# Kernel tuning notes

Hardware: AMD Instinct MI355X
Metric: run time of the kernel (lower is better)

Reference implementation:

```python
import jax, jax.numpy as jnp
import numpy as np
from jax import lax

B, N, T, H, E, D, K = 2, 1024, 4096, 256, 2, 2, 9


def angle2vector(a):
    return jnp.stack([jnp.sin(a), jnp.cos(a)], axis=-1)


def setup_inputs() -> dict:
    key = jax.random.key(0)
    ks = jax.random.split(key, 16)
    s = jnp.float32(0.05)
    return {
        "x": jax.random.normal(ks[0], (B, N, T), jnp.float32),
        "z": jax.random.uniform(ks[1], (B, T, E, D), jnp.float32, 0.0, 2.0 * np.pi),
        # encoder: depthwise conv (groups=N) then two 1x1 convs
        "dw_w": jax.random.normal(ks[2], (N, 1, K), jnp.float32) * s,
        "dw_b": jax.random.normal(ks[3], (N,), jnp.float32) * s,
        "w1": jax.random.normal(ks[4], (H, N), jnp.float32) * s,
        "b1": jax.random.normal(ks[5], (H,), jnp.float32) * s,
        "w2": jax.random.normal(ks[6], (H, H), jnp.float32) * s,
        "b2": jax.random.normal(ks[7], (H,), jnp.float32) * s,
        # heads (1x1 convs)
        "wm": jax.random.normal(ks[8], (E * D * 2, H), jnp.float32) * s,
        "bm": jax.random.normal(ks[9], (E * D * 2,), jnp.float32) * s,
        "wv": jax.random.normal(ks[10], (E * D, H), jnp.float32) * s,
        "bv": jax.random.normal(ks[11], (E * D,), jnp.float32) * s,
        # feature basis / readout params
        "receptive_fields": jax.random.uniform(ks[12], (N, E, D), jnp.float32, 0.0, 2.0 * np.pi),
        "ensemble_weights": jax.random.normal(ks[13], (N, E), jnp.float32),
        "final_scale": jax.random.normal(ks[14], (N,), jnp.float32) * s,
        "log_tuning_width": jnp.full((1,), np.log(2.0), jnp.float32),
    }


def reference(x, z, dw_w, dw_b, w1, b1, w2, b2, wm, bm, wv, bv,
              receptive_fields, ensemble_weights, final_scale, log_tuning_width):
    # ---- encoder ----
    # depthwise conv1d, kernel_size=K, padding='same', groups=N
    h = lax.conv_general_dilated(
        x, dw_w, window_strides=(1,), padding="SAME",
        feature_group_count=N, dimension_numbers=("NCH", "OIH", "NCH"))
    h = h + dw_b[None, :, None]
    h = jax.nn.relu(jnp.einsum("hn,bnt->bht", w1, h) + b1[None, :, None])
    h = jax.nn.relu(jnp.einsum("gh,bht->bgt", w2, h) + b2[None, :, None])

    # ---- heads ----
    mu = jnp.einsum("oh,bht->bot", wm, h) + bm[None, :, None]  # [B, E*D*2, T]
    mu = mu.transpose(0, 2, 1).reshape(B, T, E, D, 2)
    logvar = jnp.einsum("oh,bht->bot", wv, h) + bv[None, :, None]  # [B, E*D, T]
    logvar = logvar.transpose(0, 2, 1).reshape(B, T, E, D)
    # normalize encodings onto unit circle
    mu = mu / jnp.sqrt(jnp.sum(mu ** 2, axis=-1, keepdims=True))

    # ---- feature basis ('bump') ----
    zv = angle2vector(z)                     # [B, T, E, D, 2]
    rfv = angle2vector(receptive_fields)     # [N, E, D, 2]
    diff = zv[:, :, None] - rfv[None, None]  # [B, T, N, E, D, 2]
    dist = jnp.sum(diff ** 2, axis=(4, 5))   # [B, T, N, E]
    response = jnp.exp(-dist / jnp.exp(log_tuning_width))  # nonlinearity='exp'

    # ---- ensemble-weighted readout ----
    ew = jax.nn.softmax(ensemble_weights, axis=1)  # [N, E]
    responses = jnp.einsum("btne,ne->btn", response, ew)
    responses = responses * jnp.exp(final_scale)[None, None]
    responses = responses.transpose(0, 2, 1)  # [B, N, T]
    return responses, z, mu, logvar
```

## Files before the change

### kernel.cpp

```cpp
#include <hip/hip_runtime.h>
#include <hip/hip_bf16.h>

#define B_ 2
#define N_ 1024
#define T_ 4096
#define H_ 256
#define ROWS_ 8192

typedef float f32x4 __attribute__((ext_vector_type(4)));
typedef __bf16 bf16x8 __attribute__((ext_vector_type(8)));

__device__ __forceinline__ void gl16(const void* g, void* l) {
  __builtin_amdgcn_global_load_lds(
      (const __attribute__((address_space(1))) void*)g,
      (__attribute__((address_space(3))) void*)l, 16, 0, 0);
}

__global__ __launch_bounds__(256) void cvt_split(
    const float* __restrict__ w1, const float* __restrict__ w2,
    __bf16* __restrict__ w1h, __bf16* __restrict__ w1l,
    __bf16* __restrict__ w2h, __bf16* __restrict__ w2l) {
  int i = blockIdx.x * 256 + threadIdx.x;
  if (i < 262144) {
    float v = w1[i];
    __bf16 h = (__bf16)v;
    w1h[i] = h;
    w1l[i] = (__bf16)(v - (float)h);
  } else {
    int j = i - 262144;
    float v = w2[j];
    __bf16 h = (__bf16)v;
    w2h[j] = h;
    w2l[j] = (__bf16)(v - (float)h);
  }
}

__global__ __launch_bounds__(256) void dwconv_t(
    const float* __restrict__ x, const float* __restrict__ w,
    const float* __restrict__ bias, __bf16* __restrict__ h0h,
    __bf16* __restrict__ h0l) {
  __shared__ float xs[64][76];
  const int tid = threadIdx.x;
  const int t0 = blockIdx.x * 64;
  const int n0 = blockIdx.y * 64;
  const int b = blockIdx.z;
  for (int i = tid; i < 64 * 72; i += 256) {
    int rr = i / 72, cc = i % 72;
    int tt = t0 - 4 + cc;
    xs[rr][cc] = (tt >= 0 && tt < T_) ? x[((size_t)(b * N_ + n0 + rr)) * T_ + tt] : 0.f;
  }
  const int nl = tid & 63;
  const int tg = tid >> 6;
  float wr[9];
  #pragma unroll
  for (int k = 0; k < 9; ++k) wr[k] = w[(n0 + nl) * 9 + k];
  const float bb = bias[n0 + nl];
  __syncthreads();
  float win[24];
  #pragma unroll
  for (int c = 0; c < 6; ++c)
    *(f32x4*)&win[c * 4] = *(const f32x4*)&xs[nl][tg * 16 + c * 4];
  const size_t obase = ((size_t)b * T_ + t0 + tg * 16) * N_ + n0 + nl;
  #pragma unroll
  for (int j = 0; j < 16; ++j) {
    float acc = bb;
    #pragma unroll
    for (int k = 0; k < 9; ++k) acc = fmaf(win[j + k], wr[k], acc);
    __bf16 h = (__bf16)acc;
    h0h[obase + (size_t)j * N_] = h;
    h0l[obase + (size_t)j * N_] = (__bf16)(acc - (float)h);
  }
}

__global__ __launch_bounds__(256) void gemm3p(
    const __bf16* __restrict__ Ah, const __bf16* __restrict__ Al,
    const __bf16* __restrict__ Wh, const __bf16* __restrict__ Wl,
    const float* __restrict__ bias, __bf16* __restrict__ Oh,
    __bf16* __restrict__ Ol, int K, int relu) {
  __shared__ __bf16 As[2][2][64 * 32];
  __shared__ __bf16 Ws[2][2][64 * 32];
  const int tid = threadIdx.x;
  const int orig = blockIdx.x;
  const int rm = (orig & 7) * 64 + (orig >> 3);
  const int g0 = (rm & 3) * 64;
  const int row0 = (rm >> 2) * 64;

  const int sr = tid >> 2;
  const int sl = tid & 3;
  const int ssl = sl ^ ((sr >> 1) & 3);
  const size_t a_off = (size_t)(row0 + sr) * K + ssl * 8;
  const size_t w_off = (size_t)(g0 + sr) * K + ssl * 8;

  const int lane = tid & 63;
  const int wid = tid >> 6;
  const int wrr = (wid >> 1) * 32;
  const int wcc = (wid & 1) * 32;
  const int lr = lane & 15;
  const int ls = lane >> 4;

  f32x4 acc[2][2];
  #pragma unroll
  for (int i = 0; i < 2; ++i)
    #pragma unroll
    for (int j = 0; j < 2; ++j) acc[i][j] = (f32x4)0.f;

  auto STAGE = [&](int buf, int k0) {
    gl16(Ah + a_off + k0, &As[buf][0][tid * 8]);
    gl16(Al + a_off + k0, &As[buf][1][tid * 8]);
    gl16(Wh + w_off + k0, &Ws[buf][0][tid * 8]);
    gl16(Wl + w_off + k0, &Ws[buf][1][tid * 8]);
  };

  auto FADDR = [&](int r) { return r * 32 + (ls ^ ((r >> 1) & 3)) * 8; };

  const int nk = K >> 5;
  STAGE(0, 0);
  __syncthreads();
  for (int kt = 0; kt < nk; ++kt) {
    const int cur = kt & 1;
    if (kt + 1 < nk) STAGE(cur ^ 1, (kt + 1) << 5);
    bf16x8 ah[2], al[2], wh[2], wl[2];
    #pragma unroll
    for (int mi = 0; mi < 2; ++mi) {
      int a = FADDR(wrr + mi * 16 + lr);
      ah[mi] = *(const bf16x8*)&As[cur][0][a];
      al[mi] = *(const bf16x8*)&As[cur][1][a];
    }
    #pragma unroll
    for (int ni = 0; ni < 2; ++ni) {
      int a = FADDR(wcc + ni * 16 + lr);
      wh[ni] = *(const bf16x8*)&Ws[cur][0][a];
      wl[ni] = *(const bf16x8*)&Ws[cur][1][a];
    }
    #pragma unroll
    for (int mi = 0; mi < 2; ++mi)
      #pragma unroll
      for (int ni = 0; ni < 2; ++ni) {
        acc[mi][ni] = __builtin_amdgcn_mfma_f32_16x16x32_bf16(ah[mi], wh[ni], acc[mi][ni], 0, 0, 0);
        acc[mi][ni] = __builtin_amdgcn_mfma_f32_16x16x32_bf16(ah[mi], wl[ni], acc[mi][ni], 0, 0, 0);
        acc[mi][ni] = __builtin_amdgcn_mfma_f32_16x16x32_bf16(al[mi], wh[ni], acc[mi][ni], 0, 0, 0);
      }
    __syncthreads();
  }

  #pragma unroll
  for (int ni = 0; ni < 2; ++ni) {
    const int g = g0 + wcc + ni * 16 + lr;
    const float bb = bias[g];
    #pragma unroll
    for (int mi = 0; mi < 2; ++mi)
      #pragma unroll
      for (int reg = 0; reg < 4; ++reg) {
        int t = row0 + wrr + mi * 16 + ls * 4 + reg;
        float v = acc[mi][ni][reg] + bb;
        if (relu) v = fmaxf(v, 0.f);
        __bf16 h = (__bf16)v;
        Oh[(size_t)t * H_ + g] = h;
        Ol[(size_t)t * H_ + g] = (__bf16)(v - (float)h);
      }
  }
}

__global__ __launch_bounds__(256) void heads_t(
    const __bf16* __restrict__ h2h, const __bf16* __restrict__ h2l,
    const float* __restrict__ wm, const float* __restrict__ bm,
    const float* __restrict__ wv, const float* __restrict__ bv,
    float* __restrict__ out_mu, float* __restrict__ out_lv) {
  __shared__ float sw[12][256];
  const int tid = threadIdx.x;
  for (int i = tid; i < 8 * 256; i += 256) sw[i >> 8][i & 255] = wm[i];
  for (int i = tid; i < 4 * 256; i += 256) sw[8 + (i >> 8)][i & 255] = wv[i];
  __syncthreads();
  const int tq = tid & 3;
  const int tl = tid >> 2;
  const size_t row = blockIdx.x * 64 + tl;
  float s[12];
  #pragma unroll
  for (int o = 0; o < 12; ++o) s[o] = 0.f;
  for (int j = 0; j < 8; ++j) {
    int jj = (j + tq * 2) & 7;
    int k0 = tq * 64 + jj * 8;
    bf16x8 vh = *(const bf16x8*)&h2h[row * 256 + k0];
    bf16x8 vl = *(const bf16x8*)&h2l[row * 256 + k0];
    #pragma unroll
    for (int e = 0; e < 8; ++e) {
      float v = (float)vh[e] + (float)vl[e];
      #pragma unroll
      for (int o = 0; o < 12; ++o) s[o] = fmaf(sw[o][k0 + e], v, s[o]);
    }
  }
  #pragma unroll
  for (int o = 0; o < 12; ++o) {
    s[o] += __shfl_xor(s[o], 1);
    s[o] += __shfl_xor(s[o], 2);
  }
  if (tq == 0) {
    float mm[8];
    #pragma unroll
    for (int ed = 0; ed < 4; ++ed) {
      float m0 = s[ed * 2] + bm[ed * 2];
      float m1 = s[ed * 2 + 1] + bm[ed * 2 + 1];
      float inv = 1.f / sqrtf(m0 * m0 + m1 * m1);
      mm[ed * 2] = m0 * inv;
      mm[ed * 2 + 1] = m1 * inv;
    }
    *(float4*)&out_mu[row * 8] = make_float4(mm[0], mm[1], mm[2], mm[3]);
    *(float4*)&out_mu[row * 8 + 4] = make_float4(mm[4], mm[5], mm[6], mm[7]);
  } else if (tq == 1) {
    *(float4*)&out_lv[row * 4] =
        make_float4(s[8] + bv[0], s[9] + bv[1], s[10] + bv[2], s[11] + bv[3]);
  }
}

__global__ __launch_bounds__(256) void resp_kernel(
    const float* __restrict__ z, const float* __restrict__ rf,
    const float* __restrict__ ew, const float* __restrict__ fs,
    const float* __restrict__ ltw, float* __restrict__ out,
    float* __restrict__ out_z) {
  __shared__ float s_sin[64][4];
  __shared__ float s_cos[64][4];
  __shared__ float s_w[64][2];
  const int tid = threadIdx.x;
  const int tc = blockIdx.x;
  const int nc = blockIdx.y;
  const int b = blockIdx.z;
  {
    int nl = tid >> 2, ed = tid & 3;
    float a = rf[(nc * 64 + nl) * 4 + ed];
    s_sin[nl][ed] = sinf(a);
    s_cos[nl][ed] = cosf(a);
  }
  if (tid < 64) {
    int n = nc * 64 + tid;
    float e0 = ew[n * 2], e1 = ew[n * 2 + 1];
    float m = fmaxf(e0, e1);
    float x0 = expf(e0 - m), x1 = expf(e1 - m);
    float sc = expf(fs[n]) / (x0 + x1);
    s_w[tid][0] = x0 * sc;
    s_w[tid][1] = x1 * sc;
  }
  __syncthreads();
  const int t = tc * 256 + tid;
  const float inv_tw = expf(-ltw[0]);
  float4 zv = *(const float4*)&z[((size_t)b * T_ + t) * 4];
  if (nc == 0) *(float4*)&out_z[((size_t)b * T_ + t) * 4] = zv;
  float sz0 = sinf(zv.x), cz0 = cosf(zv.x);
  float sz1 = sinf(zv.y), cz1 = cosf(zv.y);
  float sz2 = sinf(zv.z), cz2 = cosf(zv.z);
  float sz3 = sinf(zv.w), cz3 = cosf(zv.w);
  float* op = out + (size_t)b * N_ * T_ + (size_t)(nc * 64) * T_ + t;
  #pragma unroll 4
  for (int nl = 0; nl < 64; ++nl) {
    float dot0 = sz0 * s_sin[nl][0] + cz0 * s_cos[nl][0] +
                 sz1 * s_sin[nl][1] + cz1 * s_cos[nl][1];
    float dot1 = sz2 * s_sin[nl][2] + cz2 * s_cos[nl][2] +
                 sz3 * s_sin[nl][3] + cz3 * s_cos[nl][3];
    float r0 = __expf((2.f * dot0 - 4.f) * inv_tw);
    float r1 = __expf((2.f * dot1 - 4.f) * inv_tw);
    op[(size_t)nl * T_] = s_w[nl][0] * r0 + s_w[nl][1] * r1;
  }
}

extern "C" void kernel_launch(void* const* d_in, const int* in_sizes, int n_in,
                              void* d_out, int out_size, void* d_ws, size_t ws_size,
                              hipStream_t stream) {
  const float* x   = (const float*)d_in[0];
  const float* z   = (const float*)d_in[1];
  const float* dww = (const float*)d_in[2];
  const float* dwb = (const float*)d_in[3];
  const float* w1  = (const float*)d_in[4];
  const float* b1  = (const float*)d_in[5];
  const float* w2  = (const float*)d_in[6];
  const float* b2  = (const float*)d_in[7];
  const float* wm  = (const float*)d_in[8];
  const float* bm  = (const float*)d_in[9];
  const float* wv  = (const float*)d_in[10];
  const float* bv  = (const float*)d_in[11];
  const float* rf  = (const float*)d_in[12];
  const float* ew  = (const float*)d_in[13];
  const float* fs  = (const float*)d_in[14];
  const float* ltw = (const float*)d_in[15];

  float* out = (float*)d_out;
  float* out_resp = out;
  float* out_z    = out + (size_t)B_ * N_ * T_;
  float* out_mu   = out_z + (size_t)B_ * T_ * 4;
  float* out_lv   = out_mu + (size_t)B_ * T_ * 8;

  __bf16* h0h = (__bf16*)out_resp;
  __bf16* h0l = h0h + (size_t)ROWS_ * N_;

  __bf16* p = (__bf16*)d_ws;
  __bf16* w1h = p; p += 262144;
  __bf16* w1l = p; p += 262144;
  __bf16* w2h = p; p += 65536;
  __bf16* w2l = p; p += 65536;
  __bf16* h1h = p; p += (size_t)ROWS_ * H_;
  __bf16* h1l = p; p += (size_t)ROWS_ * H_;
  __bf16* h2h = p; p += (size_t)ROWS_ * H_;
  __bf16* h2l = p; p += (size_t)ROWS_ * H_;

  cvt_split<<<1280, 256, 0, stream>>>(w1, w2, w1h, w1l, w2h, w2l);
  dwconv_t<<<dim3(T_ / 64, N_ / 64, B_), 256, 0, stream>>>(x, dww, dwb, h0h, h0l);
  gemm3p<<<dim3(512), 256, 0, stream>>>(h0h, h0l, w1h, w1l, b1, h1h, h1l, N_, 1);
  gemm3p<<<dim3(512), 256, 0, stream>>>(h1h, h1l, w2h, w2l, b2, h2h, h2l, H_, 1);
  heads_t<<<dim3(ROWS_ / 64), 256, 0, stream>>>(
      h2h, h2l, wm, bm, wv, bv, out_mu, out_lv);
  resp_kernel<<<dim3(T_ / 256, N_ / 64, B_), 256, 0, stream>>>(
      z, rf, ew, fs, ltw, out_resp, out_z);
}
```

Before: 183.0 us.

## Fuse both encoder GEMMs and heads into one kernel; vectorize response stores

After: 186.4 us. No clear change (+1.9%).

```diff
diff --git a/kernel.cpp b/kernel.cpp
--- a/kernel.cpp
+++ b/kernel.cpp
@@ -72,129 +72,170 @@
   }
 }
 
-__global__ __launch_bounds__(256) void gemm3p(
+__global__ __launch_bounds__(512) void encoder_fused(
     const __bf16* __restrict__ Ah, const __bf16* __restrict__ Al,
-    const __bf16* __restrict__ Wh, const __bf16* __restrict__ Wl,
-    const float* __restrict__ bias, __bf16* __restrict__ Oh,
-    __bf16* __restrict__ Ol, int K, int relu) {
-  __shared__ __bf16 As[2][2][64 * 32];
-  __shared__ __bf16 Ws[2][2][64 * 32];
-  const int tid = threadIdx.x;
-  const int orig = blockIdx.x;
-  const int rm = (orig & 7) * 64 + (orig >> 3);
-  const int g0 = (rm & 3) * 64;
-  const int row0 = (rm >> 2) * 64;
-
-  const int sr = tid >> 2;
-  const int sl = tid & 3;
-  const int ssl = sl ^ ((sr >> 1) & 3);
-  const size_t a_off = (size_t)(row0 + sr) * K + ssl * 8;
-  const size_t w_off = (size_t)(g0 + sr) * K + ssl * 8;
-
-  const int lane = tid & 63;
-  const int wid = tid >> 6;
-  const int wrr = (wid >> 1) * 32;
-  const int wcc = (wid & 1) * 32;
-  const int lr = lane & 15;
-  const int ls = lane >> 4;
-
-  f32x4 acc[2][2];
-  #pragma unroll
-  for (int i = 0; i < 2; ++i)
-    #pragma unroll
-    for (int j = 0; j < 2; ++j) acc[i][j] = (f32x4)0.f;
-
-  auto STAGE = [&](int buf, int k0) {
-    gl16(Ah + a_off + k0, &As[buf][0][tid * 8]);
-    gl16(Al + a_off + k0, &As[buf][1][tid * 8]);
-    gl16(Wh + w_off + k0, &Ws[buf][0][tid * 8]);
-    gl16(Wl + w_off + k0, &Ws[buf][1][tid * 8]);
-  };
-
-  auto FADDR = [&](int r) { return r * 32 + (ls ^ ((r >> 1) & 3)) * 8; };
-
-  const int nk = K >> 5;
-  STAGE(0, 0);
-  __syncthreads();
-  for (int kt = 0; kt < nk; ++kt) {
-    const int cur = kt & 1;
-    if (kt + 1 < nk) STAGE(cur ^ 1, (kt + 1) << 5);
-    bf16x8 ah[2], al[2], wh[2], wl[2];
-    #pragma unroll
-    for (int mi = 0; mi < 2; ++mi) {
-      int a = FADDR(wrr + mi * 16 + lr);
-      ah[mi] = *(const bf16x8*)&As[cur][0][a];
-      al[mi] = *(const bf16x8*)&As[cur][1][a];
-    }
-    #pragma unroll
-    for (int ni = 0; ni < 2; ++ni) {
-      int a = FADDR(wcc + ni * 16 + lr);
-      wh[ni] = *(const bf16x8*)&Ws[cur][0][a];
-      wl[ni] = *(const bf16x8*)&Ws[cur][1][a];
-    }
-    #pragma unroll
-    for (int mi = 0; mi < 2; ++mi)
-      #pragma unroll
-      for (int ni = 0; ni < 2; ++ni) {
-        acc[mi][ni] = __builtin_amdgcn_mfma_f32_16x16x32_bf16(ah[mi], wh[ni], acc[mi][ni], 0, 0, 0);
-        acc[mi][ni] = __builtin_amdgcn_mfma_f32_16x16x32_bf16(ah[mi], wl[ni], acc[mi][ni], 0, 0, 0);
-        acc[mi][ni] = __builtin_amdgcn_mfma_f32_16x16x32_bf16(al[mi], wh[ni], acc[mi][ni], 0, 0, 0);
-      }
-    __syncthreads();
-  }
-
-  #pragma unroll
-  for (int ni = 0; ni < 2; ++ni) {
-    const int g = g0 + wcc + ni * 16 + lr;
-    const float bb = bias[g];
-    #pragma unroll
-    for (int mi = 0; mi < 2; ++mi)
-      #pragma unroll
-      for (int reg = 0; reg < 4; ++reg) {
-        int t = row0 + wrr + mi * 16 + ls * 4 + reg;
-        float v = acc[mi][ni][reg] + bb;
-        if (relu) v = fmaxf(v, 0.f);
-        __bf16 h = (__bf16)v;
-        Oh[(size_t)t * H_ + g] = h;
-        Ol[(size_t)t * H_ + g] = (__bf16)(v - (float)h);
-      }
-  }
-}
-
-__global__ __launch_bounds__(256) void heads_t(
-    const __bf16* __restrict__ h2h, const __bf16* __restrict__ h2l,
+    const __bf16* __restrict__ W1h, const __bf16* __restrict__ W1l,
+    const float* __restrict__ b1,
+    const __bf16* __restrict__ W2h, const __bf16* __restrict__ W2l,
+    const float* __restrict__ b2,
     const float* __restrict__ wm, const float* __restrict__ bm,
     const float* __restrict__ wv, const float* __restrict__ bv,
     float* __restrict__ out_mu, float* __restrict__ out_lv) {
-  __shared__ float sw[12][256];
+  __shared__ __attribute__((aligned(16))) char smem[126976];
+  char* const ASB = smem;
+  char* const WSB = smem + 8192;
+  char* const H1B = smem + 73728;
+  float* const WMV = (float*)(smem + 106496);
+  float* const H2S = (float*)(smem + 8192);
+
   const int tid = threadIdx.x;
-  for (int i = tid; i < 8 * 256; i += 256) sw[i >> 8][i & 255] = wm[i];
-  for (int i = tid; i < 4 * 256; i += 256) sw[8 + (i >> 8)][i & 255] = wv[i];
-  __syncthreads();
-  const int tq = tid & 3;
-  const int tl = tid >> 2;
-  const size_t row = blockIdx.x * 64 + tl;
+  const int row0 = blockIdx.x * 32;
+  const int lane = tid & 63;
+  const int wid = tid >> 6;
+  const int wt = (wid >> 2) * 16;
+  const int wg = (wid & 3) * 64;
+  const int lr = lane & 15;
+  const int ls = lane >> 4;
+
+  if (tid < 256) {
+    #pragma unroll
+    for (int i = 0; i < 8; ++i) WMV[tid * 20 + i] = wm[i * 256 + tid];
+    #pragma unroll
+    for (int i = 0; i < 4; ++i) WMV[tid * 20 + 8 + i] = wv[i * 256 + tid];
+  }
+
+  float b1g[4], b2g[4];
+  #pragma unroll
+  for (int ni = 0; ni < 4; ++ni) {
+    b1g[ni] = b1[wg + ni * 16 + lr];
+    b2g[ni] = b2[wg + ni * 16 + lr];
+  }
+
+  const int a_pl = tid >> 7;
+  const int a_idx = tid & 127;
+  const int a_r = a_idx >> 2;
+  const int a_c = (a_idx & 3) ^ ((a_r >> 1) & 3);
+  const __bf16* a_src = (a_pl ? Al : Ah) + (size_t)(row0 + a_r) * 1024 + a_c * 8;
+  char* const a_dst = ASB + a_pl * 2048 + a_idx * 16;
+
+  auto STAGE_A = [&](int buf, int kt) {
+    if (tid < 256) gl16(a_src + kt * 32, a_dst + buf * 4096);
+  };
+  auto STAGE_W = [&](int buf, int k0, const __bf16* Wh, const __bf16* Wl, int K) {
+    #pragma unroll
+    for (int j = 0; j < 4; ++j) {
+      const int s = tid + j * 512;
+      const int pl = s >> 10;
+      const int idx = s & 1023;
+      const int g = idx >> 2;
+      const int c = (idx & 3) ^ ((g >> 1) & 3);
+      gl16((pl ? Wl : Wh) + (size_t)g * K + k0 + c * 8, WSB + buf * 32768 + s * 16);
+    }
+  };
+  auto FR_A = [&](int cur, int pl, int r) {
+    return *(const bf16x8*)(ASB + cur * 4096 + pl * 2048 + r * 64 +
+                            (ls ^ ((r >> 1) & 3)) * 16);
+  };
+  auto FR_W = [&](int cur, int pl, int g) {
+    return *(const bf16x8*)(WSB + cur * 32768 + pl * 16384 + g * 64 +
+                            (ls ^ ((g >> 1) & 3)) * 16);
+  };
+
+  f32x4 acc[4];
+  #pragma unroll
+  for (int i = 0; i < 4; ++i) acc[i] = (f32x4)0.f;
+
+  STAGE_A(0, 0);
+  STAGE_W(0, 0, W1h, W1l, 1024);
+  __syncthreads();
+  for (int kt = 0; kt < 32; ++kt) {
+    const int cur = kt & 1;
+    if (kt + 1 < 32) {
+      STAGE_A(cur ^ 1, kt + 1);
+      STAGE_W(cur ^ 1, (kt + 1) * 32, W1h, W1l, 1024);
+    }
+    bf16x8 ah = FR_A(cur, 0, wt + lr);
+    bf16x8 al = FR_A(cur, 1, wt + lr);
+    #pragma unroll
+    for (int ni = 0; ni < 4; ++ni) {
+      bf16x8 wh = FR_W(cur, 0, wg + ni * 16 + lr);
+      bf16x8 wl = FR_W(cur, 1, wg + ni * 16 + lr);
+      acc[ni] = __builtin_amdgcn_mfma_f32_16x16x32_bf16(ah, wh, acc[ni], 0, 0, 0);
+      acc[ni] = __builtin_amdgcn_mfma_f32_16x16x32_bf16(ah, wl, acc[ni], 0, 0, 0);
+      acc[ni] = __builtin_amdgcn_mfma_f32_16x16x32_bf16(al, wh, acc[ni], 0, 0, 0);
+    }
+    __syncthreads();
+  }
+
+  #pragma unroll
+  for (int ni = 0; ni < 4; ++ni) {
+    const int g = wg + ni * 16 + lr;
+    const int c = g >> 3;
+    #pragma unroll
+    for (int reg = 0; reg < 4; ++reg) {
+      const int t = wt + ls * 4 + reg;
+      float v = fmaxf(acc[ni][reg] + b1g[ni], 0.f);
+      __bf16 h = (__bf16)v;
+      const int off = t * 512 + ((c ^ (t & 7)) * 16) + (g & 7) * 2;
+      *(__bf16*)(H1B + off) = h;
+      *(__bf16*)(H1B + 16384 + off) = (__bf16)(v - (float)h);
+    }
+    acc[ni] = (f32x4)0.f;
+  }
+  STAGE_W(0, 0, W2h, W2l, 256);
+  __syncthreads();
+
+  for (int kt = 0; kt < 8; ++kt) {
+    const int cur = kt & 1;
+    if (kt + 1 < 8) STAGE_W(cur ^ 1, (kt + 1) * 32, W2h, W2l, 256);
+    const int t = wt + lr;
+    const int ca = ((kt * 4 + ls) ^ (t & 7)) * 16;
+    bf16x8 ah = *(const bf16x8*)(H1B + t * 512 + ca);
+    bf16x8 al = *(const bf16x8*)(H1B + 16384 + t * 512 + ca);
+    #pragma unroll
+    for (int ni = 0; ni < 4; ++ni) {
+      bf16x8 wh = FR_W(cur, 0, wg + ni * 16 + lr);
+      bf16x8 wl = FR_W(cur, 1, wg + ni * 16 + lr);
+      acc[ni] = __builtin_amdgcn_mfma_f32_16x16x32_bf16(ah, wh, acc[ni], 0, 0, 0);
+      acc[ni] = __builtin_amdgcn_mfma_f32_16x16x32_bf16(ah, wl, acc[ni], 0, 0, 0);
+      acc[ni] = __builtin_amdgcn_mfma_f32_16x16x32_bf16(al, wh, acc[ni], 0, 0, 0);
+    }
+    __syncthreads();
+  }
+
+  #pragma unroll
+  for (int ni = 0; ni < 4; ++ni) {
+    const int g = wg + ni * 16 + lr;
+    #pragma unroll
+    for (int reg = 0; reg < 4; ++reg) {
+      const int t = wt + ls * 4 + reg;
+      H2S[t * 264 + g] = fmaxf(acc[ni][reg] + b2g[ni], 0.f);
+    }
+  }
+  __syncthreads();
+
+  const int ht = tid >> 4;
+  const int sub = tid & 15;
   float s[12];
   #pragma unroll
   for (int o = 0; o < 12; ++o) s[o] = 0.f;
-  for (int j = 0; j < 8; ++j) {
-    int jj = (j + tq * 2) & 7;
-    int k0 = tq * 64 + jj * 8;
-    bf16x8 vh = *(const bf16x8*)&h2h[row * 256 + k0];
-    bf16x8 vl = *(const bf16x8*)&h2l[row * 256 + k0];
-    #pragma unroll
-    for (int e = 0; e < 8; ++e) {
-      float v = (float)vh[e] + (float)vl[e];
-      #pragma unroll
-      for (int o = 0; o < 12; ++o) s[o] = fmaf(sw[o][k0 + e], v, s[o]);
-    }
+  #pragma unroll
+  for (int j = 0; j < 16; ++j) {
+    const int k = sub + j * 16;
+    const float hv = H2S[ht * 264 + k];
+    const float* wp = &WMV[k * 20];
+    #pragma unroll
+    for (int o = 0; o < 12; ++o) s[o] = fmaf(wp[o], hv, s[o]);
   }
   #pragma unroll
   for (int o = 0; o < 12; ++o) {
     s[o] += __shfl_xor(s[o], 1);
     s[o] += __shfl_xor(s[o], 2);
-  }
-  if (tq == 0) {
+    s[o] += __shfl_xor(s[o], 4);
+    s[o] += __shfl_xor(s[o], 8);
+  }
+  const size_t row = row0 + ht;
+  if (sub == 0) {
     float mm[8];
     #pragma unroll
     for (int ed = 0; ed < 4; ++ed) {
@@ -206,7 +247,7 @@
     }
     *(float4*)&out_mu[row * 8] = make_float4(mm[0], mm[1], mm[2], mm[3]);
     *(float4*)&out_mu[row * 8 + 4] = make_float4(mm[4], mm[5], mm[6], mm[7]);
-  } else if (tq == 1) {
+  } else if (sub == 1) {
     *(float4*)&out_lv[row * 4] =
         make_float4(s[8] + bv[0], s[9] + bv[1], s[10] + bv[2], s[11] + bv[3]);
   }
@@ -217,21 +258,19 @@
     const float* __restrict__ ew, const float* __restrict__ fs,
     const float* __restrict__ ltw, float* __restrict__ out,
     float* __restrict__ out_z) {
-  __shared__ float s_sin[64][4];
-  __shared__ float s_cos[64][4];
-  __shared__ float s_w[64][2];
+  __shared__ float s_sin[32][4], s_cos[32][4], s_w[32][2];
   const int tid = threadIdx.x;
   const int tc = blockIdx.x;
   const int nc = blockIdx.y;
   const int b = blockIdx.z;
-  {
+  if (tid < 128) {
     int nl = tid >> 2, ed = tid & 3;
-    float a = rf[(nc * 64 + nl) * 4 + ed];
+    float a = rf[(nc * 32 + nl) * 4 + ed];
     s_sin[nl][ed] = sinf(a);
     s_cos[nl][ed] = cosf(a);
   }
-  if (tid < 64) {
-    int n = nc * 64 + tid;
+  if (tid < 32) {
+    int n = nc * 32 + tid;
     float e0 = ew[n * 2], e1 = ew[n * 2 + 1];
     float m = fmaxf(e0, e1);
     float x0 = expf(e0 - m), x1 = expf(e1 - m);
@@ -240,24 +279,35 @@
     s_w[tid][1] = x1 * sc;
   }
   __syncthreads();
-  const int t = tc * 256 + tid;
+  const int t = tc * 1024 + (tid >> 6) * 256 + (tid & 63) * 4;
   const float inv_tw = expf(-ltw[0]);
-  float4 zv = *(const float4*)&z[((size_t)b * T_ + t) * 4];
-  if (nc == 0) *(float4*)&out_z[((size_t)b * T_ + t) * 4] = zv;
-  float sz0 = sinf(zv.x), cz0 = cosf(zv.x);
-  float sz1 = sinf(zv.y), cz1 = cosf(zv.y);
-  float sz2 = sinf(zv.z), cz2 = cosf(zv.z);
-  float sz3 = sinf(zv.w), cz3 = cosf(zv.w);
-  float* op = out + (size_t)b * N_ * T_ + (size_t)(nc * 64) * T_ + t;
-  #pragma unroll 4
-  for (int nl = 0; nl < 64; ++nl) {
-    float dot0 = sz0 * s_sin[nl][0] + cz0 * s_cos[nl][0] +
-                 sz1 * s_sin[nl][1] + cz1 * s_cos[nl][1];
-    float dot1 = sz2 * s_sin[nl][2] + cz2 * s_cos[nl][2] +
-                 sz3 * s_sin[nl][3] + cz3 * s_cos[nl][3];
-    float r0 = __expf((2.f * dot0 - 4.f) * inv_tw);
-    float r1 = __expf((2.f * dot1 - 4.f) * inv_tw);
-    op[(size_t)nl * T_] = s_w[nl][0] * r0 + s_w[nl][1] * r1;
+  float sz[16], cz[16];
+  #pragma unroll
+  for (int j = 0; j < 4; ++j) {
+    float4 zv = *(const float4*)&z[((size_t)b * T_ + t + j) * 4];
+    if (nc == 0) *(float4*)&out_z[((size_t)b * T_ + t + j) * 4] = zv;
+    sz[j * 4 + 0] = sinf(zv.x); cz[j * 4 + 0] = cosf(zv.x);
+    sz[j * 4 + 1] = sinf(zv.y); cz[j * 4 + 1] = cosf(zv.y);
+    sz[j * 4 + 2] = sinf(zv.z); cz[j * 4 + 2] = cosf(zv.z);
+    sz[j * 4 + 3] = sinf(zv.w); cz[j * 4 + 3] = cosf(zv.w);
+  }
+  float* op = out + (size_t)b * N_ * T_ + (size_t)(nc * 32) * T_ + t;
+  for (int nl = 0; nl < 32; ++nl) {
+    const float ss0 = s_sin[nl][0], sc0 = s_cos[nl][0];
+    const float ss1 = s_sin[nl][1], sc1 = s_cos[nl][1];
+    const float ss2 = s_sin[nl][2], sc2 = s_cos[nl][2];
+    const float ss3 = s_sin[nl][3], sc3 = s_cos[nl][3];
+    const float w0 = s_w[nl][0], w1 = s_w[nl][1];
+    float o[4];
+    #pragma unroll
+    for (int j = 0; j < 4; ++j) {
+      float d0 = sz[j * 4] * ss0 + cz[j * 4] * sc0 + sz[j * 4 + 1] * ss1 + cz[j * 4 + 1] * sc1;
+      float d1 = sz[j * 4 + 2] * ss2 + cz[j * 4 + 2] * sc2 + sz[j * 4 + 3] * ss3 + cz[j * 4 + 3] * sc3;
+      float r0 = __expf((2.f * d0 - 4.f) * inv_tw);
+      float r1 = __expf((2.f * d1 - 4.f) * inv_tw);
+      o[j] = w0 * r0 + w1 * r1;
+    }
+    *(float4*)&op[(size_t)nl * T_] = make_float4(o[0], o[1], o[2], o[3]);
   }
 }
 
@@ -295,17 +345,11 @@
   __bf16* w1l = p; p += 262144;
   __bf16* w2h = p; p += 65536;
   __bf16* w2l = p; p += 65536;
-  __bf16* h1h = p; p += (size_t)ROWS_ * H_;
-  __bf16* h1l = p; p += (size_t)ROWS_ * H_;
-  __bf16* h2h = p; p += (size_t)ROWS_ * H_;
-  __bf16* h2l = p; p += (size_t)ROWS_ * H_;
 
   cvt_split<<<1280, 256, 0, stream>>>(w1, w2, w1h, w1l, w2h, w2l);
   dwconv_t<<<dim3(T_ / 64, N_ / 64, B_), 256, 0, stream>>>(x, dww, dwb, h0h, h0l);
-  gemm3p<<<dim3(512), 256, 0, stream>>>(h0h, h0l, w1h, w1l, b1, h1h, h1l, N_, 1);
-  gemm3p<<<dim3(512), 256, 0, stream>>>(h1h, h1l, w2h, w2l, b2, h2h, h2l, H_, 1);
-  heads_t<<<dim3(ROWS_ / 64), 256, 0, stream>>>(
-      h2h, h2l, wm, bm, wv, bv, out_mu, out_lv);
-  resp_kernel<<<dim3(T_ / 256, N_ / 64, B_), 256, 0, stream>>>(
+  encoder_fused<<<dim3(ROWS_ / 32), 512, 0, stream>>>(
+      h0h, h0l, w1h, w1l, b1, w2h, w2l, b2, wm, bm, wv, bv, out_mu, out_lv);
+  resp_kernel<<<dim3(4, 32, 2), 256, 0, stream>>>(
       z, rf, ew, fs, ltw, out_resp, out_z);
 }
```
